# Kernel tuning notes

Hardware: AMD Instinct MI355X
Metric: run time of the kernel (lower is better)

## Reference

```python
import jax, jax.numpy as jnp
import numpy as np

D_MODEL = 1024
NUM_HEADS = 16
THETA = 10000.0
B, T = 2, 2048


def _rope(x, pos, theta_base):
    # x: (b, h, t, d_h); interleaved pairs (x0,x1),(x2,x3),... per the
    # rearrange '... (c d) -> ... c d' with d=2 in the original module.
    d = x.shape[-1]
    half = d // 2
    inv_freq = 1.0 / (theta_base ** (2.0 * jnp.arange(half, dtype=jnp.float32) / d))
    ang = pos.astype(jnp.float32)[:, None] * inv_freq[None, :]  # (t, half)
    sin = jnp.sin(ang)[None, None]  # (1,1,t,half)
    cos = jnp.cos(ang)[None, None]
    x1 = x[..., 0::2]
    x2 = x[..., 1::2]
    r1 = x1 * cos - x2 * sin
    r2 = x1 * sin + x2 * cos
    return jnp.stack([r1, r2], axis=-1).reshape(x.shape)


def setup_inputs() -> dict:
    key = jax.random.key(0)
    k0, k1, k2, k3, k4 = jax.random.split(key, 5)
    sigma = (2.0 / (D_MODEL + D_MODEL)) ** 0.5
    return {
        "in_features": jax.random.normal(k0, (B, T, D_MODEL), dtype=jnp.float32),
        "Wq": jax.random.normal(k1, (D_MODEL, D_MODEL), dtype=jnp.float32) * sigma,
        "Wk": jax.random.normal(k2, (D_MODEL, D_MODEL), dtype=jnp.float32) * sigma,
        "Wv": jax.random.normal(k3, (D_MODEL, D_MODEL), dtype=jnp.float32) * sigma,
        "Wo": jax.random.normal(k4, (D_MODEL, D_MODEL), dtype=jnp.float32) * sigma,
        "token_positions": jnp.arange(T, dtype=jnp.int32),
    }


def reference(in_features, Wq, Wk, Wv, Wo, token_positions):
    b, t, d_model = in_features.shape
    h = NUM_HEADS
    d_h = d_model // h
    # Fused-style QKV projections (x @ W.T, weights stored (in, out))
    q = in_features @ Wq.T
    k = in_features @ Wk.T
    v = in_features @ Wv.T
    # (b, t, h*d_h) -> (b, h, t, d_h)
    q = q.reshape(b, t, h, d_h).transpose(0, 2, 1, 3)
    k = k.reshape(b, t, h, d_h).transpose(0, 2, 1, 3)
    v = v.reshape(b, t, h, d_h).transpose(0, 2, 1, 3)
    q = _rope(q, token_positions, THETA)
    k = _rope(k, token_positions, THETA)
    scale = 1.0 / jnp.sqrt(jnp.asarray(d_h, dtype=q.dtype))
    scores = jnp.einsum('bhqd,bhkd->bhqk', q, k) * scale
    causal = jnp.tril(jnp.ones((t, t), dtype=bool))
    scores = jnp.where(causal[None, None], scores, -jnp.inf)
    attn = jax.nn.softmax(scores, axis=-1)
    out = jnp.einsum('bhqk,bhkd->bhqd', attn, v)
    out = out.transpose(0, 2, 1, 3).reshape(b, t, h * d_h)
    return out @ Wo.T
```

## Files before the change

kernel.cpp:

```cpp
#include <hip/hip_runtime.h>

#define D_MODEL 1024
#define NUM_HEADS 16
#define DH 64
#define B_SZ 2
#define T_SZ 2048
#define M_ROWS (B_SZ * T_SZ)

typedef __bf16 bf16;
typedef __bf16 bf16x4 __attribute__((ext_vector_type(4)));
typedef __bf16 bf16x8 __attribute__((ext_vector_type(8)));
typedef float f32x4 __attribute__((ext_vector_type(4)));

__device__ __forceinline__ void async_copy16(const bf16* g, bf16* l) {
  __builtin_amdgcn_global_load_lds(
      (const __attribute__((address_space(1))) void*)g,
      (__attribute__((address_space(3))) void*)l, 16, 0, 0);
}

#define NX (M_ROWS * D_MODEL / 4)
#define NW (D_MODEL * D_MODEL / 4)

__global__ __launch_bounds__(256) void cast_all(
    const float* __restrict__ X, const float* __restrict__ Wq,
    const float* __restrict__ Wk, const float* __restrict__ Wv,
    const float* __restrict__ Wo,
    bf16* __restrict__ Xb, bf16* __restrict__ Wqb, bf16* __restrict__ Wkb,
    bf16* __restrict__ Wvb, bf16* __restrict__ Wob) {
  int i = blockIdx.x * 256 + threadIdx.x;
  const float* s; bf16* d; int off;
  if (i < NX) {
    s = X; d = Xb; off = i;
  } else {
    int j = i - NX;
    int w = j >> 18;
    off = j & (NW - 1);
    if (w == 0)      { s = Wq; d = Wqb; }
    else if (w == 1) { s = Wk; d = Wkb; }
    else if (w == 2) { s = Wv; d = Wvb; }
    else             { s = Wo; d = Wob; }
  }
  float4 v = ((const float4*)s)[off];
  bf16x4 o;
  o[0] = (bf16)v.x; o[1] = (bf16)v.y; o[2] = (bf16)v.z; o[3] = (bf16)v.w;
  ((bf16x4*)d)[off] = o;
}

__global__ __launch_bounds__(256) void qkv_gemm(
    const bf16* __restrict__ Xb,
    const bf16* __restrict__ Wqb, const bf16* __restrict__ Wkb,
    const bf16* __restrict__ Wvb,
    bf16* __restrict__ Q, bf16* __restrict__ K, bf16* __restrict__ V) {
  __shared__ bf16 As[128 * 32];
  __shared__ bf16 Bs[128 * 32];

  int tid = threadIdx.x;
  int wave = tid >> 6, lane = tid & 63;
  int wm = wave >> 1, wn = wave & 1;
  int l15 = lane & 15, quad = lane >> 4;

  int row0 = blockIdx.x * 128;
  int col0 = blockIdx.y * 128;
  int sel = col0 >> 10;
  int nb = col0 & 1023;
  const bf16* W; bf16* Out;
  if (sel == 0)      { W = Wqb; Out = Q; }
  else if (sel == 1) { W = Wkb; Out = K; }
  else               { W = Wvb; Out = V; }

  int srow = tid >> 2;
  int schunk = tid & 3;
  const bf16* Ag = Xb + (size_t)(row0 + srow) * D_MODEL + schunk * 8;
  const bf16* Bg = W + (size_t)(nb + srow) * D_MODEL + schunk * 8;
  bf16* Al0 = &As[srow * 32 + schunk * 8];
  bf16* Al1 = &As[(srow + 64) * 32 + schunk * 8];
  bf16* Bl0 = &Bs[srow * 32 + schunk * 8];
  bf16* Bl1 = &Bs[(srow + 64) * 32 + schunk * 8];

  f32x4 acc[4][4];
#pragma unroll
  for (int i = 0; i < 4; ++i)
#pragma unroll
    for (int j = 0; j < 4; ++j) acc[i][j] = (f32x4){0.f, 0.f, 0.f, 0.f};

  for (int k0 = 0; k0 < D_MODEL; k0 += 32) {
    async_copy16(Ag + k0, Al0);
    async_copy16(Ag + k0 + (size_t)64 * D_MODEL, Al1);
    async_copy16(Bg + k0, Bl0);
    async_copy16(Bg + k0 + (size_t)64 * D_MODEL, Bl1);
    __syncthreads();

    bf16x8 af[4], bfr[4];
#pragma unroll
    for (int i = 0; i < 4; ++i)
      af[i] = *(const bf16x8*)&As[(wm * 64 + i * 16 + l15) * 32 + quad * 8];
#pragma unroll
    for (int j = 0; j < 4; ++j)
      bfr[j] = *(const bf16x8*)&Bs[(wn * 64 + j * 16 + l15) * 32 + quad * 8];
#pragma unroll
    for (int i = 0; i < 4; ++i)
#pragma unroll
      for (int j = 0; j < 4; ++j)
        acc[i][j] = __builtin_amdgcn_mfma_f32_16x16x32_bf16(af[i], bfr[j],
                                                            acc[i][j], 0, 0, 0);
    __syncthreads();
  }

#pragma unroll
  for (int i = 0; i < 4; ++i) {
    int row = row0 + wm * 64 + i * 16 + quad * 4;
#pragma unroll
    for (int j = 0; j < 4; ++j) {
      int col = nb + wn * 64 + j * 16 + l15;
#pragma unroll
      for (int r = 0; r < 4; ++r)
        Out[(size_t)(row + r) * D_MODEL + col] = (bf16)acc[i][j][r];
    }
  }
}

#define ROPEK_BLOCKS (M_ROWS * NUM_HEADS * 32 / 256)

__global__ __launch_bounds__(256) void ropek_vt(
    bf16* __restrict__ K, const bf16* __restrict__ V, bf16* __restrict__ VT,
    const int* __restrict__ pos) {
  int b0 = blockIdx.x;
  if (b0 < ROPEK_BLOCKS) {
    int idx = b0 * 256 + threadIdx.x;
    int i = idx & 31;
    int h = (idx >> 5) & 15;
    int row = idx >> 9;
    int t = row & (T_SZ - 1);
    float p = (float)pos[t];
    float freq = __expf(-(float)i * 0.28782313662425f);
    float s, c;
    sincosf(p * freq, &s, &c);
    size_t base = (size_t)row * D_MODEL + h * DH + 2 * i;
    float k1 = (float)K[base], k2 = (float)K[base + 1];
    K[base]     = (bf16)(k1 * c - k2 * s);
    K[base + 1] = (bf16)(k1 * s + k2 * c);
  } else {
    __shared__ bf16 tile[64][72];
    int vb = b0 - ROPEK_BLOCKS;
    int bh = vb >> 5;
    int tt = vb & 31;
    int b = bh >> 4, h = bh & 15;
    int tid = threadIdx.x;
    int rr = tid >> 3;
    int cc = (tid & 7) * 8;
#pragma unroll
    for (int p = 0; p < 2; ++p) {
      int t = rr + p * 32;
      bf16x8 v = *(const bf16x8*)&V[((size_t)b * T_SZ + tt * 64 + t) * D_MODEL +
                                    h * DH + cc];
      *(bf16x8*)&tile[t][cc] = v;
    }
    __syncthreads();
#pragma unroll
    for (int p = 0; p < 2; ++p) {
      int d = rr + p * 32;
      bf16x8 o;
#pragma unroll
      for (int j = 0; j < 8; ++j) o[j] = tile[cc + j][d];
      *(bf16x8*)&VT[((size_t)bh * DH + d) * T_SZ + tt * 64 + cc] = o;
    }
  }
}

#define PST 72
#define KST 72

__global__ __launch_bounds__(256) void attn_kernel(
    const bf16* __restrict__ Q, const bf16* __restrict__ K,
    const bf16* __restrict__ VT, const int* __restrict__ pos,
    bf16* __restrict__ AO) {
  __shared__ bf16 Kt[64 * KST];
  __shared__ bf16 Vt[64 * KST];
  __shared__ bf16 Pbuf[4][16 * PST];

  int bh = blockIdx.x;
  int qi = 31 - (int)blockIdx.y;
  int bb = bh >> 4, h = bh & 15;
  int tid = threadIdx.x;
  int wave = tid >> 6, lane = tid & 63;
  int l15 = lane & 15, quad = lane >> 4;

  int q0 = qi * 64 + wave * 16;
  size_t grow = (size_t)bb * T_SZ + q0;

  const bf16* Qp = Q + (grow + l15) * D_MODEL + h * DH + quad * 8;
  bf16x8 bq0 = *(const bf16x8*)(Qp);
  bf16x8 bq1 = *(const bf16x8*)(Qp + 32);
  {
    float p = (float)pos[q0 + l15];
#pragma unroll
    for (int jj = 0; jj < 4; ++jj) {
      int i0 = quad * 4 + jj;
      float s, c;
      sincosf(p * __expf(-(float)i0 * 0.28782313662425f), &s, &c);
      float x1 = (float)bq0[2 * jj], x2 = (float)bq0[2 * jj + 1];
      bq0[2 * jj]     = (bf16)(x1 * c - x2 * s);
      bq0[2 * jj + 1] = (bf16)(x1 * s + x2 * c);
      sincosf(p * __expf(-(float)(i0 + 16) * 0.28782313662425f), &s, &c);
      float y1 = (float)bq1[2 * jj], y2 = (float)bq1[2 * jj + 1];
      bq1[2 * jj]     = (bf16)(y1 * c - y2 * s);
      bq1[2 * jj + 1] = (bf16)(y1 * s + y2 * c);
    }
  }

  f32x4 o[4];
#pragma unroll
  for (int nt = 0; nt < 4; ++nt) o[nt] = (f32x4){0.f, 0.f, 0.f, 0.f};
  float l_i = 0.f;

  int srow = tid >> 2;
  int sc = (tid & 3) * 16;
  const bf16* Kg = K + ((size_t)bb * T_SZ + srow) * D_MODEL + h * DH + sc;
  const bf16* Vg = VT + ((size_t)bh * DH + srow) * T_SZ + sc;
  bf16* Kl = &Kt[srow * KST + sc];
  bf16* Vl = &Vt[srow * KST + sc];

  bf16* Pw = Pbuf[wave];
  int nchunks = qi + 1;
  int rel = wave * 16 + l15;

  bf16x8 kr0 = *(const bf16x8*)(Kg);
  bf16x8 kr1 = *(const bf16x8*)(Kg + 8);
  bf16x8 vr0 = *(const bf16x8*)(Vg);
  bf16x8 vr1 = *(const bf16x8*)(Vg + 8);

  for (int t = 0; t < nchunks; ++t) {
    __syncthreads();
    *(bf16x8*)(Kl) = kr0;
    *(bf16x8*)(Kl + 8) = kr1;
    *(bf16x8*)(Vl) = vr0;
    *(bf16x8*)(Vl + 8) = vr1;
    if (t + 1 < nchunks) {
      const bf16* Kn = Kg + (size_t)(t + 1) * 64 * D_MODEL;
      const bf16* Vn = Vg + (t + 1) * 64;
      kr0 = *(const bf16x8*)(Kn);
      kr1 = *(const bf16x8*)(Kn + 8);
      vr0 = *(const bf16x8*)(Vn);
      vr1 = *(const bf16x8*)(Vn + 8);
    }
    __syncthreads();

    f32x4 st[4];
#pragma unroll
    for (int cs = 0; cs < 4; ++cs) {
      bf16x8 ak0 = *(const bf16x8*)&Kt[(cs * 16 + l15) * KST + quad * 8];
      bf16x8 ak1 = *(const bf16x8*)&Kt[(cs * 16 + l15) * KST + 32 + quad * 8];
      f32x4 s4 = (f32x4){0.f, 0.f, 0.f, 0.f};
      s4 = __builtin_amdgcn_mfma_f32_16x16x32_bf16(ak0, bq0, s4, 0, 0, 0);
      s4 = __builtin_amdgcn_mfma_f32_16x16x32_bf16(ak1, bq1, s4, 0, 0, 0);
      st[cs] = s4;
    }

    bool last = (t == nchunks - 1);
    float ps = 0.f;
#pragma unroll
    for (int cs = 0; cs < 4; ++cs)
#pragma unroll
      for (int r = 0; r < 4; ++r) {
        float p = __expf(st[cs][r] * 0.125f);
        if (last) {
          int cl = cs * 16 + quad * 4 + r;
          p = (cl > rel) ? 0.f : p;
        }
        st[cs][r] = p;
        ps += p;
      }
    l_i += ps;

#pragma unroll
    for (int cs = 0; cs < 4; ++cs) {
      bf16x4 pk;
#pragma unroll
      for (int r = 0; r < 4; ++r) pk[r] = (bf16)st[cs][r];
      *(bf16x4*)&Pw[l15 * PST + cs * 16 + quad * 4] = pk;
    }
    __asm__ __volatile__("" ::: "memory");
    bf16x8 bp0 = *(const bf16x8*)&Pw[l15 * PST + quad * 8];
    bf16x8 bp1 = *(const bf16x8*)&Pw[l15 * PST + 32 + quad * 8];
    __asm__ __volatile__("" ::: "memory");

#pragma unroll
    for (int nt = 0; nt < 4; ++nt) {
      bf16x8 av0 = *(const bf16x8*)&Vt[(nt * 16 + l15) * KST + quad * 8];
      bf16x8 av1 = *(const bf16x8*)&Vt[(nt * 16 + l15) * KST + 32 + quad * 8];
      o[nt] = __builtin_amdgcn_mfma_f32_16x16x32_bf16(av0, bp0, o[nt], 0, 0, 0);
      o[nt] = __builtin_amdgcn_mfma_f32_16x16x32_bf16(av1, bp1, o[nt], 0, 0, 0);
    }
  }

  l_i += __shfl_xor(l_i, 16);
  l_i += __shfl_xor(l_i, 32);
  float inv = 1.0f / l_i;
#pragma unroll
  for (int nt = 0; nt < 4; ++nt) {
    bf16x4 ov;
#pragma unroll
    for (int r = 0; r < 4; ++r) ov[r] = (bf16)(o[nt][r] * inv);
    *(bf16x4*)&AO[(grow + l15) * D_MODEL + h * DH + nt * 16 + quad * 4] = ov;
  }
}

__global__ __launch_bounds__(256) void out_gemm(
    const bf16* __restrict__ AO, const bf16* __restrict__ Wob,
    float* __restrict__ out) {
  __shared__ bf16 As[128 * 32];
  __shared__ bf16 Bs[64 * 32];

  int tid = threadIdx.x;
  int wave = tid >> 6, lane = tid & 63;
  int l15 = lane & 15, quad = lane >> 4;

  int row0 = blockIdx.x * 128;
  int nb = blockIdx.y * 64;

  int srow = tid >> 2;
  int schunk = tid & 3;
  const bf16* Ag = AO + (size_t)(row0 + srow) * D_MODEL + schunk * 8;
  const bf16* Bg = Wob + (size_t)(nb + srow) * D_MODEL + schunk * 8;
  bf16* Al0 = &As[srow * 32 + schunk * 8];
  bf16* Al1 = &As[(srow + 64) * 32 + schunk * 8];
  bf16* Bl = &Bs[srow * 32 + schunk * 8];

  f32x4 acc[2][4];
#pragma unroll
  for (int i = 0; i < 2; ++i)
#pragma unroll
    for (int j = 0; j < 4; ++j) acc[i][j] = (f32x4){0.f, 0.f, 0.f, 0.f};

  for (int k0 = 0; k0 < D_MODEL; k0 += 32) {
    async_copy16(Ag + k0, Al0);
    async_copy16(Ag + k0 + (size_t)64 * D_MODEL, Al1);
    async_copy16(Bg + k0, Bl);
    __syncthreads();

    bf16x8 af[2], bfr[4];
#pragma unroll
    for (int i = 0; i < 2; ++i)
      af[i] = *(const bf16x8*)&As[(wave * 32 + i * 16 + l15) * 32 + quad * 8];
#pragma unroll
    for (int j = 0; j < 4; ++j)
      bfr[j] = *(const bf16x8*)&Bs[(j * 16 + l15) * 32 + quad * 8];
#pragma unroll
    for (int i = 0; i < 2; ++i)
#pragma unroll
      for (int j = 0; j < 4; ++j)
        acc[i][j] = __builtin_amdgcn_mfma_f32_16x16x32_bf16(af[i], bfr[j],
                                                            acc[i][j], 0, 0, 0);
    __syncthreads();
  }

#pragma unroll
  for (int i = 0; i < 2; ++i) {
    int row = row0 + wave * 32 + i * 16 + quad * 4;
#pragma unroll
    for (int j = 0; j < 4; ++j) {
      int col = nb + j * 16 + l15;
#pragma unroll
      for (int r = 0; r < 4; ++r)
        out[(size_t)(row + r) * D_MODEL + col] = acc[i][j][r];
    }
  }
}

extern "C" void kernel_launch(void* const* d_in, const int* in_sizes, int n_in,
                              void* d_out, int out_size, void* d_ws, size_t ws_size,
                              hipStream_t stream) {
  const float* X  = (const float*)d_in[0];
  const float* Wq = (const float*)d_in[1];
  const float* Wk = (const float*)d_in[2];
  const float* Wv = (const float*)d_in[3];
  const float* Wo = (const float*)d_in[4];
  const int*  pos = (const int*)d_in[5];
  float* out = (float*)d_out;

  char* w = (char*)d_ws;
  bf16* Xb  = (bf16*)w;  w += (size_t)M_ROWS * D_MODEL * 2;
  bf16* Wqb = (bf16*)w;  w += (size_t)D_MODEL * D_MODEL * 2;
  bf16* Wkb = (bf16*)w;  w += (size_t)D_MODEL * D_MODEL * 2;
  bf16* Wvb = (bf16*)w;  w += (size_t)D_MODEL * D_MODEL * 2;
  bf16* Wob = (bf16*)w;  w += (size_t)D_MODEL * D_MODEL * 2;
  bf16* Qb  = (bf16*)w;  w += (size_t)M_ROWS * D_MODEL * 2;
  bf16* Kb  = (bf16*)w;  w += (size_t)M_ROWS * D_MODEL * 2;
  bf16* Vb  = (bf16*)w;  w += (size_t)M_ROWS * D_MODEL * 2;
  bf16* AO  = (bf16*)w;  w += (size_t)M_ROWS * D_MODEL * 2;
  bf16* VT  = (bf16*)w;  w += (size_t)M_ROWS * D_MODEL * 2;

  cast_all<<<(NX + 4 * NW) / 256, 256, 0, stream>>>(X, Wq, Wk, Wv, Wo,
                                                    Xb, Wqb, Wkb, Wvb, Wob);
  qkv_gemm<<<dim3(M_ROWS / 128, 3 * D_MODEL / 128), 256, 0, stream>>>(
      Xb, Wqb, Wkb, Wvb, Qb, Kb, Vb);
  ropek_vt<<<ROPEK_BLOCKS + B_SZ * NUM_HEADS * (T_SZ / 64), 256, 0, stream>>>(
      Kb, Vb, VT, pos);
  attn_kernel<<<dim3(B_SZ * NUM_HEADS, T_SZ / 64), 256, 0, stream>>>(
      Qb, Kb, VT, pos, AO);
  out_gemm<<<dim3(M_ROWS / 128, D_MODEL / 64), 256, 0, stream>>>(AO, Wob, out);
}
```

Baseline: 184.0 us.

## Process 128 query rows per attention block to reuse K/V tiles across two subtiles

Each wave now handles 32 query rows, as two 16-row subtiles, so a block covers 128 queries instead of 64. Each K/V chunk staged in LDS feeds twice as many MFMAs, which halves global and LDS traffic for K/V per query and halves the grid size. Chunks fully above the causal diagonal for a wave are skipped, and masking is applied on the last two chunks. The cost is more registers per thread, fewer blocks to balance the causal workload across CUs, and some idle waves on diagonal chunks.

```diff
diff --git a/kernel.cpp b/kernel.cpp
--- a/kernel.cpp
+++ b/kernel.cpp
@@ -176,53 +176,59 @@
     bf16* __restrict__ AO) {
   __shared__ bf16 Kt[64 * KST];
   __shared__ bf16 Vt[64 * KST];
-  __shared__ bf16 Pbuf[4][16 * PST];
+  __shared__ bf16 Pbuf[4][2][16 * PST];
 
   int bh = blockIdx.x;
-  int qi = 31 - (int)blockIdx.y;
+  int qi = (T_SZ / 128 - 1) - (int)blockIdx.y;
   int bb = bh >> 4, h = bh & 15;
   int tid = threadIdx.x;
   int wave = tid >> 6, lane = tid & 63;
   int l15 = lane & 15, quad = lane >> 4;
 
-  int q0 = qi * 64 + wave * 16;
-  size_t grow = (size_t)bb * T_SZ + q0;
-
-  const bf16* Qp = Q + (grow + l15) * D_MODEL + h * DH + quad * 8;
-  bf16x8 bq0 = *(const bf16x8*)(Qp);
-  bf16x8 bq1 = *(const bf16x8*)(Qp + 32);
-  {
-    float p = (float)pos[q0 + l15];
+  int q0 = qi * 128 + wave * 32;
+  size_t growb = (size_t)bb * T_SZ;
+
+  bf16x8 bq[2][2];
+#pragma unroll
+  for (int s = 0; s < 2; ++s) {
+    const bf16* Qp =
+        Q + (growb + q0 + s * 16 + l15) * D_MODEL + h * DH + quad * 8;
+    bq[s][0] = *(const bf16x8*)(Qp);
+    bq[s][1] = *(const bf16x8*)(Qp + 32);
+    float p = (float)pos[q0 + s * 16 + l15];
 #pragma unroll
     for (int jj = 0; jj < 4; ++jj) {
       int i0 = quad * 4 + jj;
-      float s, c;
-      sincosf(p * __expf(-(float)i0 * 0.28782313662425f), &s, &c);
-      float x1 = (float)bq0[2 * jj], x2 = (float)bq0[2 * jj + 1];
-      bq0[2 * jj]     = (bf16)(x1 * c - x2 * s);
-      bq0[2 * jj + 1] = (bf16)(x1 * s + x2 * c);
-      sincosf(p * __expf(-(float)(i0 + 16) * 0.28782313662425f), &s, &c);
-      float y1 = (float)bq1[2 * jj], y2 = (float)bq1[2 * jj + 1];
-      bq1[2 * jj]     = (bf16)(y1 * c - y2 * s);
-      bq1[2 * jj + 1] = (bf16)(y1 * s + y2 * c);
-    }
-  }
-
-  f32x4 o[4];
-#pragma unroll
-  for (int nt = 0; nt < 4; ++nt) o[nt] = (f32x4){0.f, 0.f, 0.f, 0.f};
-  float l_i = 0.f;
+      float sn, cn;
+      sincosf(p * __expf(-(float)i0 * 0.28782313662425f), &sn, &cn);
+      float x1 = (float)bq[s][0][2 * jj], x2 = (float)bq[s][0][2 * jj + 1];
+      bq[s][0][2 * jj]     = (bf16)(x1 * cn - x2 * sn);
+      bq[s][0][2 * jj + 1] = (bf16)(x1 * sn + x2 * cn);
+      sincosf(p * __expf(-(float)(i0 + 16) * 0.28782313662425f), &sn, &cn);
+      float y1 = (float)bq[s][1][2 * jj], y2 = (float)bq[s][1][2 * jj + 1];
+      bq[s][1][2 * jj]     = (bf16)(y1 * cn - y2 * sn);
+      bq[s][1][2 * jj + 1] = (bf16)(y1 * sn + y2 * cn);
+    }
+  }
+
+  f32x4 o[2][4];
+#pragma unroll
+  for (int s = 0; s < 2; ++s)
+#pragma unroll
+    for (int nt = 0; nt < 4; ++nt) o[s][nt] = (f32x4){0.f, 0.f, 0.f, 0.f};
+  float l_i[2] = {0.f, 0.f};
 
   int srow = tid >> 2;
   int sc = (tid & 3) * 16;
-  const bf16* Kg = K + ((size_t)bb * T_SZ + srow) * D_MODEL + h * DH + sc;
+  const bf16* Kg = K + (growb + srow) * D_MODEL + h * DH + sc;
   const bf16* Vg = VT + ((size_t)bh * DH + srow) * T_SZ + sc;
   bf16* Kl = &Kt[srow * KST + sc];
   bf16* Vl = &Vt[srow * KST + sc];
 
-  bf16* Pw = Pbuf[wave];
-  int nchunks = qi + 1;
-  int rel = wave * 16 + l15;
+  bf16* Pw0 = Pbuf[wave][0];
+  bf16* Pw1 = Pbuf[wave][1];
+  int nchunks = 2 * (qi + 1);
+  int qlast = q0 + 31;
 
   bf16x8 kr0 = *(const bf16x8*)(Kg);
   bf16x8 kr1 = *(const bf16x8*)(Kg + 8);
@@ -245,63 +251,95 @@
     }
     __syncthreads();
 
-    f32x4 st[4];
-#pragma unroll
-    for (int cs = 0; cs < 4; ++cs) {
-      bf16x8 ak0 = *(const bf16x8*)&Kt[(cs * 16 + l15) * KST + quad * 8];
-      bf16x8 ak1 = *(const bf16x8*)&Kt[(cs * 16 + l15) * KST + 32 + quad * 8];
-      f32x4 s4 = (f32x4){0.f, 0.f, 0.f, 0.f};
-      s4 = __builtin_amdgcn_mfma_f32_16x16x32_bf16(ak0, bq0, s4, 0, 0, 0);
-      s4 = __builtin_amdgcn_mfma_f32_16x16x32_bf16(ak1, bq1, s4, 0, 0, 0);
-      st[cs] = s4;
-    }
-
-    bool last = (t == nchunks - 1);
-    float ps = 0.f;
-#pragma unroll
-    for (int cs = 0; cs < 4; ++cs)
-#pragma unroll
-      for (int r = 0; r < 4; ++r) {
-        float p = __expf(st[cs][r] * 0.125f);
-        if (last) {
-          int cl = cs * 16 + quad * 4 + r;
-          p = (cl > rel) ? 0.f : p;
+    if (t * 64 <= qlast) {
+      bf16x8 ak[4][2];
+#pragma unroll
+      for (int cs = 0; cs < 4; ++cs) {
+        ak[cs][0] = *(const bf16x8*)&Kt[(cs * 16 + l15) * KST + quad * 8];
+        ak[cs][1] = *(const bf16x8*)&Kt[(cs * 16 + l15) * KST + 32 + quad * 8];
+      }
+
+      f32x4 st[2][4];
+#pragma unroll
+      for (int s = 0; s < 2; ++s)
+#pragma unroll
+        for (int cs = 0; cs < 4; ++cs) {
+          f32x4 s4 = (f32x4){0.f, 0.f, 0.f, 0.f};
+          s4 = __builtin_amdgcn_mfma_f32_16x16x32_bf16(ak[cs][0], bq[s][0], s4,
+                                                       0, 0, 0);
+          s4 = __builtin_amdgcn_mfma_f32_16x16x32_bf16(ak[cs][1], bq[s][1], s4,
+                                                       0, 0, 0);
+          st[s][cs] = s4;
         }
-        st[cs][r] = p;
-        ps += p;
+
+      bool maskc = (t >= nchunks - 2);
+#pragma unroll
+      for (int s = 0; s < 2; ++s) {
+        int rel = q0 + s * 16 + l15 - t * 64;
+        float ps = 0.f;
+#pragma unroll
+        for (int cs = 0; cs < 4; ++cs)
+#pragma unroll
+          for (int r = 0; r < 4; ++r) {
+            float p = __expf(st[s][cs][r] * 0.125f);
+            if (maskc) {
+              int cl = cs * 16 + quad * 4 + r;
+              p = (cl > rel) ? 0.f : p;
+            }
+            st[s][cs][r] = p;
+            ps += p;
+          }
+        l_i[s] += ps;
       }
-    l_i += ps;
-
-#pragma unroll
-    for (int cs = 0; cs < 4; ++cs) {
-      bf16x4 pk;
-#pragma unroll
-      for (int r = 0; r < 4; ++r) pk[r] = (bf16)st[cs][r];
-      *(bf16x4*)&Pw[l15 * PST + cs * 16 + quad * 4] = pk;
-    }
-    __asm__ __volatile__("" ::: "memory");
-    bf16x8 bp0 = *(const bf16x8*)&Pw[l15 * PST + quad * 8];
-    bf16x8 bp1 = *(const bf16x8*)&Pw[l15 * PST + 32 + quad * 8];
-    __asm__ __volatile__("" ::: "memory");
-
+
+#pragma unroll
+      for (int cs = 0; cs < 4; ++cs) {
+        bf16x4 pk0, pk1;
+#pragma unroll
+        for (int r = 0; r < 4; ++r) {
+          pk0[r] = (bf16)st[0][cs][r];
+          pk1[r] = (bf16)st[1][cs][r];
+        }
+        *(bf16x4*)&Pw0[l15 * PST + cs * 16 + quad * 4] = pk0;
+        *(bf16x4*)&Pw1[l15 * PST + cs * 16 + quad * 4] = pk1;
+      }
+      __asm__ __volatile__("" ::: "memory");
+      bf16x8 bp[2][2];
+      bp[0][0] = *(const bf16x8*)&Pw0[l15 * PST + quad * 8];
+      bp[0][1] = *(const bf16x8*)&Pw0[l15 * PST + 32 + quad * 8];
+      bp[1][0] = *(const bf16x8*)&Pw1[l15 * PST + quad * 8];
+      bp[1][1] = *(const bf16x8*)&Pw1[l15 * PST + 32 + quad * 8];
+      __asm__ __volatile__("" ::: "memory");
+
+#pragma unroll
+      for (int nt = 0; nt < 4; ++nt) {
+        bf16x8 av0 = *(const bf16x8*)&Vt[(nt * 16 + l15) * KST + quad * 8];
+        bf16x8 av1 = *(const bf16x8*)&Vt[(nt * 16 + l15) * KST + 32 + quad * 8];
+#pragma unroll
+        for (int s = 0; s < 2; ++s) {
+          o[s][nt] = __builtin_amdgcn_mfma_f32_16x16x32_bf16(av0, bp[s][0],
+                                                             o[s][nt], 0, 0, 0);
+          o[s][nt] = __builtin_amdgcn_mfma_f32_16x16x32_bf16(av1, bp[s][1],
+                                                             o[s][nt], 0, 0, 0);
+        }
+      }
+    }
+  }
+
+#pragma unroll
+  for (int s = 0; s < 2; ++s) {
+    float l = l_i[s];
+    l += __shfl_xor(l, 16);
+    l += __shfl_xor(l, 32);
+    float inv = 1.0f / l;
 #pragma unroll
     for (int nt = 0; nt < 4; ++nt) {
-      bf16x8 av0 = *(const bf16x8*)&Vt[(nt * 16 + l15) * KST + quad * 8];
-      bf16x8 av1 = *(const bf16x8*)&Vt[(nt * 16 + l15) * KST + 32 + quad * 8];
-      o[nt] = __builtin_amdgcn_mfma_f32_16x16x32_bf16(av0, bp0, o[nt], 0, 0, 0);
-      o[nt] = __builtin_amdgcn_mfma_f32_16x16x32_bf16(av1, bp1, o[nt], 0, 0, 0);
-    }
-  }
-
-  l_i += __shfl_xor(l_i, 16);
-  l_i += __shfl_xor(l_i, 32);
-  float inv = 1.0f / l_i;
-#pragma unroll
-  for (int nt = 0; nt < 4; ++nt) {
-    bf16x4 ov;
-#pragma unroll
-    for (int r = 0; r < 4; ++r) ov[r] = (bf16)(o[nt][r] * inv);
-    *(bf16x4*)&AO[(grow + l15) * D_MODEL + h * DH + nt * 16 + quad * 4] = ov;
+      bf16x4 ov;
+#pragma unroll
+      for (int r = 0; r < 4; ++r) ov[r] = (bf16)(o[s][nt][r] * inv);
+      *(bf16x4*)&AO[(growb + q0 + s * 16 + l15) * D_MODEL + h * DH + nt * 16 +
+                    quad * 4] = ov;
+    }
   }
 }
 
@@ -396,7 +434,7 @@
       Xb, Wqb, Wkb, Wvb, Qb, Kb, Vb);
   ropek_vt<<<ROPEK_BLOCKS + B_SZ * NUM_HEADS * (T_SZ / 64), 256, 0, stream>>>(
       Kb, Vb, VT, pos);
-  attn_kernel<<<dim3(B_SZ * NUM_HEADS, T_SZ / 64), 256, 0, stream>>>(
+  attn_kernel<<<dim3(B_SZ * NUM_HEADS, T_SZ / 128), 256, 0, stream>>>(
       Qb, Kb, VT, pos, AO);
   out_gemm<<<dim3(M_ROWS / 128, D_MODEL / 64), 256, 0, stream>>>(AO, Wob, out);
 }
```

Result: slower. 196.0 us (+6.5%).

## Fuse RoPE on K and V transpose into QKV GEMM epilogue

Applied to the files above, without the earlier changes.

Removes the separate ropek_vt kernel. K rotation now happens in the QKV GEMM epilogue, using a lane shuffle to pair each interleaved element with its neighbour, and V is written straight into the transposed VT layout with 4-element vector stores. sincosf is also swapped for the faster, lower-precision __sincosf in both the epilogue and the Q rotation in attention. This saves one launch plus a full read-modify-write of K and a read/write pass over V. The cost is extra transcendental work in the GEMM epilogue, strided VT stores, and reduced accuracy in the sin/cos values.

```diff
diff --git a/kernel.cpp b/kernel.cpp
--- a/kernel.cpp
+++ b/kernel.cpp
@@ -46,11 +46,13 @@
   ((bf16x4*)d)[off] = o;
 }
 
+#define KLN 0.28782313662425f
+
 __global__ __launch_bounds__(256) void qkv_gemm(
     const bf16* __restrict__ Xb,
     const bf16* __restrict__ Wqb, const bf16* __restrict__ Wkb,
-    const bf16* __restrict__ Wvb,
-    bf16* __restrict__ Q, bf16* __restrict__ K, bf16* __restrict__ V) {
+    const bf16* __restrict__ Wvb, const int* __restrict__ pos,
+    bf16* __restrict__ Q, bf16* __restrict__ K, bf16* __restrict__ VT) {
   __shared__ bf16 As[128 * 32];
   __shared__ bf16 Bs[128 * 32];
 
@@ -63,10 +65,10 @@
   int col0 = blockIdx.y * 128;
   int sel = col0 >> 10;
   int nb = col0 & 1023;
-  const bf16* W; bf16* Out;
-  if (sel == 0)      { W = Wqb; Out = Q; }
-  else if (sel == 1) { W = Wkb; Out = K; }
-  else               { W = Wvb; Out = V; }
+  const bf16* W;
+  if (sel == 0)      W = Wqb;
+  else if (sel == 1) W = Wkb;
+  else               W = Wvb;
 
   int srow = tid >> 2;
   int schunk = tid & 3;
@@ -106,63 +108,60 @@
     __syncthreads();
   }
 
-#pragma unroll
-  for (int i = 0; i < 4; ++i) {
-    int row = row0 + wm * 64 + i * 16 + quad * 4;
+  if (sel == 1) {
+    float pv[4][4];
+#pragma unroll
+    for (int i = 0; i < 4; ++i)
+#pragma unroll
+      for (int r = 0; r < 4; ++r)
+        pv[i][r] =
+            (float)pos[(row0 + wm * 64 + i * 16 + quad * 4 + r) & (T_SZ - 1)];
+    bool even = (l15 & 1) == 0;
 #pragma unroll
     for (int j = 0; j < 4; ++j) {
-      int col = nb + wn * 64 + j * 16 + l15;
-#pragma unroll
-      for (int r = 0; r < 4; ++r)
-        Out[(size_t)(row + r) * D_MODEL + col] = (bf16)acc[i][j][r];
-    }
-  }
-}
-
-#define ROPEK_BLOCKS (M_ROWS * NUM_HEADS * 32 / 256)
-
-__global__ __launch_bounds__(256) void ropek_vt(
-    bf16* __restrict__ K, const bf16* __restrict__ V, bf16* __restrict__ VT,
-    const int* __restrict__ pos) {
-  int b0 = blockIdx.x;
-  if (b0 < ROPEK_BLOCKS) {
-    int idx = b0 * 256 + threadIdx.x;
-    int i = idx & 31;
-    int h = (idx >> 5) & 15;
-    int row = idx >> 9;
-    int t = row & (T_SZ - 1);
-    float p = (float)pos[t];
-    float freq = __expf(-(float)i * 0.28782313662425f);
-    float s, c;
-    sincosf(p * freq, &s, &c);
-    size_t base = (size_t)row * D_MODEL + h * DH + 2 * i;
-    float k1 = (float)K[base], k2 = (float)K[base + 1];
-    K[base]     = (bf16)(k1 * c - k2 * s);
-    K[base + 1] = (bf16)(k1 * s + k2 * c);
+      float fr = __expf(-(float)((j * 16 + (l15 & 14)) >> 1) * KLN);
+#pragma unroll
+      for (int i = 0; i < 4; ++i)
+#pragma unroll
+        for (int r = 0; r < 4; ++r) {
+          float v = acc[i][j][r];
+          float pn = __shfl_xor(v, 1);
+          float s, c;
+          __sincosf(pv[i][r] * fr, &s, &c);
+          acc[i][j][r] = even ? (v * c - pn * s) : (pn * s + v * c);
+        }
+    }
+  }
+
+  if (sel == 2) {
+    int b = row0 >> 11;
+    int t0 = row0 & (T_SZ - 1);
+#pragma unroll
+    for (int i = 0; i < 4; ++i) {
+      int t = t0 + wm * 64 + i * 16 + quad * 4;
+#pragma unroll
+      for (int j = 0; j < 4; ++j) {
+        int col = nb + wn * 64 + j * 16 + l15;
+        int h = col >> 6;
+        int d = col & 63;
+        bf16x4 ov;
+#pragma unroll
+        for (int r = 0; r < 4; ++r) ov[r] = (bf16)acc[i][j][r];
+        *(bf16x4*)&VT[((size_t)(b * NUM_HEADS + h) * DH + d) * T_SZ + t] = ov;
+      }
+    }
   } else {
-    __shared__ bf16 tile[64][72];
-    int vb = b0 - ROPEK_BLOCKS;
-    int bh = vb >> 5;
-    int tt = vb & 31;
-    int b = bh >> 4, h = bh & 15;
-    int tid = threadIdx.x;
-    int rr = tid >> 3;
-    int cc = (tid & 7) * 8;
-#pragma unroll
-    for (int p = 0; p < 2; ++p) {
-      int t = rr + p * 32;
-      bf16x8 v = *(const bf16x8*)&V[((size_t)b * T_SZ + tt * 64 + t) * D_MODEL +
-                                    h * DH + cc];
-      *(bf16x8*)&tile[t][cc] = v;
-    }
-    __syncthreads();
-#pragma unroll
-    for (int p = 0; p < 2; ++p) {
-      int d = rr + p * 32;
-      bf16x8 o;
-#pragma unroll
-      for (int j = 0; j < 8; ++j) o[j] = tile[cc + j][d];
-      *(bf16x8*)&VT[((size_t)bh * DH + d) * T_SZ + tt * 64 + cc] = o;
+    bf16* Out = (sel == 0) ? Q : K;
+#pragma unroll
+    for (int i = 0; i < 4; ++i) {
+      int row = row0 + wm * 64 + i * 16 + quad * 4;
+#pragma unroll
+      for (int j = 0; j < 4; ++j) {
+        int col = nb + wn * 64 + j * 16 + l15;
+#pragma unroll
+        for (int r = 0; r < 4; ++r)
+          Out[(size_t)(row + r) * D_MODEL + col] = (bf16)acc[i][j][r];
+      }
     }
   }
 }
@@ -197,11 +196,11 @@
     for (int jj = 0; jj < 4; ++jj) {
       int i0 = quad * 4 + jj;
       float s, c;
-      sincosf(p * __expf(-(float)i0 * 0.28782313662425f), &s, &c);
+      __sincosf(p * __expf(-(float)i0 * KLN), &s, &c);
       float x1 = (float)bq0[2 * jj], x2 = (float)bq0[2 * jj + 1];
       bq0[2 * jj]     = (bf16)(x1 * c - x2 * s);
       bq0[2 * jj + 1] = (bf16)(x1 * s + x2 * c);
-      sincosf(p * __expf(-(float)(i0 + 16) * 0.28782313662425f), &s, &c);
+      __sincosf(p * __expf(-(float)(i0 + 16) * KLN), &s, &c);
       float y1 = (float)bq1[2 * jj], y2 = (float)bq1[2 * jj + 1];
       bq1[2 * jj]     = (bf16)(y1 * c - y2 * s);
       bq1[2 * jj + 1] = (bf16)(y1 * s + y2 * c);
@@ -386,16 +385,13 @@
   bf16* Wob = (bf16*)w;  w += (size_t)D_MODEL * D_MODEL * 2;
   bf16* Qb  = (bf16*)w;  w += (size_t)M_ROWS * D_MODEL * 2;
   bf16* Kb  = (bf16*)w;  w += (size_t)M_ROWS * D_MODEL * 2;
-  bf16* Vb  = (bf16*)w;  w += (size_t)M_ROWS * D_MODEL * 2;
+  bf16* VT  = (bf16*)w;  w += (size_t)M_ROWS * D_MODEL * 2;
   bf16* AO  = (bf16*)w;  w += (size_t)M_ROWS * D_MODEL * 2;
-  bf16* VT  = (bf16*)w;  w += (size_t)M_ROWS * D_MODEL * 2;
 
   cast_all<<<(NX + 4 * NW) / 256, 256, 0, stream>>>(X, Wq, Wk, Wv, Wo,
                                                     Xb, Wqb, Wkb, Wvb, Wob);
   qkv_gemm<<<dim3(M_ROWS / 128, 3 * D_MODEL / 128), 256, 0, stream>>>(
-      Xb, Wqb, Wkb, Wvb, Qb, Kb, Vb);
-  ropek_vt<<<ROPEK_BLOCKS + B_SZ * NUM_HEADS * (T_SZ / 64), 256, 0, stream>>>(
-      Kb, Vb, VT, pos);
+      Xb, Wqb, Wkb, Wvb, pos, Qb, Kb, VT);
   attn_kernel<<<dim3(B_SZ * NUM_HEADS, T_SZ / 64), 256, 0, stream>>>(
       Qb, Kb, VT, pos, AO);
   out_gemm<<<dim3(M_ROWS / 128, D_MODEL / 64), 256, 0, stream>>>(AO, Wob, out);
```

New measurement: 186.1 us. No clear change (+1.1%).
